# Kernel optimization log

Hardware: AMD Instinct MI355X
Metric: run time of the kernel (lower is better)

The kernel has to match this reference:

```python
import jax, jax.numpy as jnp
import numpy as np

N_NODES = 50000


def gcn_layer(x, W, b, src, dst, norm):
    # x: [N, Fin] -> [N, Fout]; PyG GCNConv: x' = D^-1/2 (A+I) D^-1/2 (x W) + b
    h = x @ W
    msg = h[src] * norm[:, None]              # gather + scale per edge (incl. self loops)
    out = jax.ops.segment_sum(msg, dst, num_segments=N_NODES)
    return out + b


def setup_inputs() -> dict:
    key = jax.random.key(0)
    ks = jax.random.split(key, 12)
    F_in, F_hid, T, E = 128, 128, 10, 1600000
    features = jax.random.normal(ks[0], (N_NODES, F_in), dtype=jnp.float32)
    edges = jax.random.randint(ks[1], (2, E), 0, N_NODES, dtype=jnp.int64)
    s = 1.0 / np.sqrt(F_in)
    W0 = jax.random.uniform(ks[2], (F_in, F_hid), jnp.float32, -s, s)
    b0 = jnp.zeros((F_hid,), jnp.float32)
    W1 = jax.random.uniform(ks[3], (F_hid, F_hid), jnp.float32, -s, s)
    b1 = jnp.zeros((F_hid,), jnp.float32)
    W2 = jax.random.uniform(ks[4], (F_hid, F_hid), jnp.float32, -s, s)
    b2 = jnp.zeros((F_hid,), jnp.float32)
    Wout = jax.random.uniform(ks[5], (F_hid, T), jnp.float32, -s, s)
    bout = jax.random.uniform(ks[6], (T,), jnp.float32, -s, s)
    return {"features": features, "edges": edges, "W0": W0, "b0": b0,
            "W1": W1, "b1": b1, "W2": W2, "b2": b2, "Wout": Wout, "bout": bout}


def reference(features, edges, W0, b0, W1, b1, W2, b2, Wout, bout):
    # Add self loops once; edge structure shared across layers.
    loop = jnp.arange(N_NODES, dtype=edges.dtype)
    src = jnp.concatenate([edges[0], loop])
    dst = jnp.concatenate([edges[1], loop])
    deg = jax.ops.segment_sum(jnp.ones_like(dst, dtype=features.dtype), dst,
                              num_segments=N_NODES)
    dinv = jnp.where(deg > 0, jax.lax.rsqrt(deg), 0.0)
    norm = dinv[src] * dinv[dst]              # [E + N]

    x = gcn_layer(features, W0, b0, src, dst, norm)
    x = gcn_layer(x, W1, b1, src, dst, norm)
    x = gcn_layer(x, W2, b2, src, dst, norm)

    pooled = jnp.mean(x, axis=0)              # [F_hid]
    logits = pooled @ Wout + bout             # [T]
    return jax.nn.log_softmax(logits, axis=0).reshape(1, -1)
```

## Files before the change

### kernel.cpp

```cpp
#include <hip/hip_runtime.h>


#define FDIM 128
#define HSZ 12500
#define NBG 64
#define NB_V0 512
#define S_FIX 16777216.0f
#define INV_S (1.0f / 16777216.0f)


__global__ void __launch_bounds__(1024)
hist_deg_kernel(const int* __restrict__ edges, int E, int e4, int N,
                int* __restrict__ partial) {
  __shared__ int h[HSZ];
  const int g = blockIdx.x / NBG;
  const int j = blockIdx.x - g * NBG;
  const int lo = g * HSZ;
  const int hi = min(N, lo + HSZ);
  const int hs = hi - lo;
  for (int i = threadIdx.x; i < hs; i += blockDim.x) h[i] = 0;
  __syncthreads();
  const int* dst = edges + E;
  const int4* dst4 = (const int4*)dst;
  for (int i = j * blockDim.x + threadIdx.x; i < e4; i += NBG * blockDim.x) {
    int4 d = dst4[i];
    if (d.x >= lo && d.x < hi) atomicAdd(&h[d.x - lo], 1);
    if (d.y >= lo && d.y < hi) atomicAdd(&h[d.y - lo], 1);
    if (d.z >= lo && d.z < hi) atomicAdd(&h[d.z - lo], 1);
    if (d.w >= lo && d.w < hi) atomicAdd(&h[d.w - lo], 1);
  }
  if (j == 0) {
    for (int e = 4 * e4 + threadIdx.x; e < E; e += blockDim.x) {
      int d = dst[e];
      if (d >= lo && d < hi) atomicAdd(&h[d - lo], 1);
    }
  }
  __syncthreads();
  int* out = partial + (size_t)blockIdx.x * HSZ;
  for (int i = threadIdx.x; i < hs; i += blockDim.x) out[i] = h[i];
}

__global__ void merge_dinv_kernel(const int* __restrict__ partial,
                                  float* __restrict__ dinv, int N) {
  int n = blockIdx.x * blockDim.x + threadIdx.x;
  if (n >= N) return;
  int g = n / HSZ;
  int off = n - g * HSZ;
  const int* p = partial + ((size_t)g * NBG) * HSZ + off;
  int s = 1;
  for (int jj = 0; jj < NBG; ++jj) s += p[(size_t)jj * HSZ];
  dinv[n] = rsqrtf((float)s);
}

__global__ void __launch_bounds__(1024)
hist_u_kernel(const int* __restrict__ edges, int E, int e4, int N,
              const float* __restrict__ w,
              float* __restrict__ partial) {
  __shared__ float h[HSZ];
  const int g = blockIdx.x / NBG;
  const int j = blockIdx.x - g * NBG;
  const int lo = g * HSZ;
  const int hi = min(N, lo + HSZ);
  const int hs = hi - lo;
  for (int i = threadIdx.x; i < hs; i += blockDim.x) h[i] = 0.f;
  __syncthreads();
  const int4* s4 = (const int4*)edges;
  const int4* d4 = (const int4*)(edges + E);
  for (int i = j * blockDim.x + threadIdx.x; i < e4; i += NBG * blockDim.x) {
    int4 s = s4[i];
    int4 d = d4[i];
    if (s.x >= lo && s.x < hi) atomicAdd(&h[s.x - lo], w[d.x]);
    if (s.y >= lo && s.y < hi) atomicAdd(&h[s.y - lo], w[d.y]);
    if (s.z >= lo && s.z < hi) atomicAdd(&h[s.z - lo], w[d.z]);
    if (s.w >= lo && s.w < hi) atomicAdd(&h[s.w - lo], w[d.w]);
  }
  if (j == 0) {
    const int* se = edges; const int* de = edges + E;
    for (int e = 4 * e4 + threadIdx.x; e < E; e += blockDim.x) {
      int s = se[e], d = de[e];
      if (s >= lo && s < hi) atomicAdd(&h[s - lo], w[d]);
    }
  }
  __syncthreads();
  float* out = partial + (size_t)blockIdx.x * HSZ;
  for (int i = threadIdx.x; i < hs; i += blockDim.x) out[i] = h[i];
}

__global__ void __launch_bounds__(256)
merge_u_kernel(const float* __restrict__ partial,
               const float* __restrict__ dinv,
               const float* __restrict__ win,
               float* __restrict__ uout,
               float* __restrict__ wout,
               float* __restrict__ ssump, int N) {
  __shared__ float red[4];
  int n = blockIdx.x * blockDim.x + threadIdx.x;
  float u = 0.f;
  if (n < N) {
    int g = n / HSZ;
    int off = n - g * HSZ;
    const float* p = partial + ((size_t)g * NBG) * HSZ + off;
    float s = 0.f;
    for (int jj = 0; jj < NBG; ++jj) s += p[(size_t)jj * HSZ];
    u = dinv[n] * (s + win[n]);
    if (uout) uout[n] = u;
    if (wout) wout[n] = dinv[n] * u;
  }
  if (ssump) {
    float a = u;
    for (int o = 32; o > 0; o >>= 1) a += __shfl_down(a, o, 64);
    if ((threadIdx.x & 63) == 0) red[threadIdx.x >> 6] = a;
    __syncthreads();
    if (threadIdx.x == 0)
      ssump[blockIdx.x] = red[0] + red[1] + red[2] + red[3];
  }
}

__global__ void v0_kernel(const float* __restrict__ feat,
                          const float* __restrict__ u0,
                          float* __restrict__ v0p, int N) {
  __shared__ float sh[2][FDIM];
  int f = threadIdx.x & (FDIM - 1);
  int r2 = threadIdx.x >> 7;
  float acc = 0.f;
  for (int r = blockIdx.x * 2 + r2; r < N; r += gridDim.x * 2)
    acc += u0[r] * feat[(size_t)r * FDIM + f];
  sh[r2][f] = acc;
  __syncthreads();
  if (r2 == 0) v0p[(size_t)blockIdx.x * FDIM + f] = sh[0][f] + sh[1][f];
}

__global__ void __launch_bounds__(1024)
final_kernel(const float* __restrict__ W0, const float* __restrict__ b0,
             const float* __restrict__ W1, const float* __restrict__ b1,
             const float* __restrict__ W2, const float* __restrict__ b2,
             const float* __restrict__ Wout, const float* __restrict__ bout,
             const float* __restrict__ v0p, int nv0,
             const float* __restrict__ ssumpA,
             const float* __restrict__ ssumpB,
             int nss,
             float* __restrict__ out, int N) {
  __shared__ float Wl[FDIM * FDIM];
  __shared__ float WoL[FDIM * 10];
  __shared__ float va[FDIM], vb[FDIM];
  __shared__ float part[8][FDIM];
  __shared__ float red0[16], red1[16];
  __shared__ float shS1, shS2;
  __shared__ float lg[10];
  const int t = threadIdx.x;
  const int f = t & (FDIM - 1);
  const int sl = t >> 7;

  {
    const float4* w4 = (const float4*)W0;
    float4* l4 = (float4*)Wl;
    #pragma unroll
    for (int i = 0; i < 4; ++i) l4[t + i * 1024] = w4[t + i * 1024];
    if (t < (FDIM * 10) / 4) ((float4*)WoL)[t] = ((const float4*)Wout)[t];
  }
  float acc = 0.f;
  for (int j = sl; j < nv0; j += 8) acc += v0p[(size_t)j * FDIM + f];
  part[sl][f] = acc;
  {
    float a0 = 0.f, a1 = 0.f;
    for (int j = t; j < nss; j += 1024) { a0 += ssumpA[j]; a1 += ssumpB[j]; }
    for (int o = 32; o > 0; o >>= 1) {
      a0 += __shfl_down(a0, o, 64);
      a1 += __shfl_down(a1, o, 64);
    }
    if ((t & 63) == 0) { red0[t >> 6] = a0; red1[t >> 6] = a1; }
  }
  __syncthreads();
  if (sl == 0) {
    float s = 0.f;
    #pragma unroll
    for (int j = 0; j < 8; ++j) s += part[j][f];
    va[f] = s;
  }
  if (t == 0) {
    float x = 0.f, y = 0.f;
    #pragma unroll
    for (int i = 0; i < 16; ++i) { x += red0[i]; y += red1[i]; }
    shS2 = x; shS1 = y;
  }
  __syncthreads();

  acc = 0.f;
  #pragma unroll
  for (int k = 0; k < 16; ++k) {
    int kk = sl * 16 + k;
    acc += va[kk] * Wl[kk * FDIM + f];
  }
  part[sl][f] = acc;
  __syncthreads();
  {
    const float4* w4 = (const float4*)W1;
    float4* l4 = (float4*)Wl;
    #pragma unroll
    for (int i = 0; i < 4; ++i) l4[t + i * 1024] = w4[t + i * 1024];
  }
  if (sl == 0) {
    float s = 0.f;
    #pragma unroll
    for (int j = 0; j < 8; ++j) s += part[j][f];
    vb[f] = s + shS1 * b0[f];
  }
  __syncthreads();

  acc = 0.f;
  #pragma unroll
  for (int k = 0; k < 16; ++k) {
    int kk = sl * 16 + k;
    acc += vb[kk] * Wl[kk * FDIM + f];
  }
  part[sl][f] = acc;
  __syncthreads();
  {
    const float4* w4 = (const float4*)W2;
    float4* l4 = (float4*)Wl;
    #pragma unroll
    for (int i = 0; i < 4; ++i) l4[t + i * 1024] = w4[t + i * 1024];
  }
  if (sl == 0) {
    float s = 0.f;
    #pragma unroll
    for (int j = 0; j < 8; ++j) s += part[j][f];
    va[f] = s + shS2 * b1[f];
  }
  __syncthreads();

  acc = 0.f;
  #pragma unroll
  for (int k = 0; k < 16; ++k) {
    int kk = sl * 16 + k;
    acc += va[kk] * Wl[kk * FDIM + f];
  }
  part[sl][f] = acc;
  __syncthreads();
  if (sl == 0) {
    float s = 0.f;
    #pragma unroll
    for (int j = 0; j < 8; ++j) s += part[j][f];
    vb[f] = s / (float)N + b2[f];
  }
  __syncthreads();

  if (t < 10) {
    float a = 0.f;
    for (int k = 0; k < FDIM; ++k) a += vb[k] * WoL[k * 10 + t];
    lg[t] = a + bout[t];
  }
  __syncthreads();
  if (t == 0) {
    float m = lg[0];
    for (int q = 1; q < 10; ++q) m = fmaxf(m, lg[q]);
    float s = 0.f;
    for (int q = 0; q < 10; ++q) s += expf(lg[q] - m);
    float lse = logf(s);
    for (int q = 0; q < 10; ++q) out[q] = lg[q] - m - lse;
  }
}


__global__ void deg_kernel(const int* __restrict__ edges, int E, int M,
                           int* __restrict__ deg) {
  for (int e = blockIdx.x * blockDim.x + threadIdx.x; e < M;
       e += gridDim.x * blockDim.x) {
    int d = (e < E) ? edges[E + e] : (e - E);
    atomicAdd(&deg[d], 1);
  }
}

__global__ void dinv_kernel(const int* __restrict__ deg,
                            float* __restrict__ dinv, int N) {
  int i = blockIdx.x * blockDim.x + threadIdx.x;
  if (i < N) {
    float d = (float)deg[i];
    dinv[i] = (d > 0.f) ? rsqrtf(d) : 0.f;
  }
}

__global__ void upass_kernel(const int* __restrict__ edges, int E, int M,
                             const float* __restrict__ dinv,
                             const int* __restrict__ uin_q,
                             int* __restrict__ uout_q) {
  for (int e = blockIdx.x * blockDim.x + threadIdx.x; e < M;
       e += gridDim.x * blockDim.x) {
    int s, d;
    if (e < E) { s = edges[e]; d = edges[E + e]; }
    else       { s = e - E;    d = s; }
    float v = dinv[s] * dinv[d];
    if (uin_q) v *= (float)uin_q[d] * INV_S;
    atomicAdd(&uout_q[s], __float2int_rn(v * S_FIX));
  }
}

__global__ void sums_kernel(const int* __restrict__ u2q,
                            const int* __restrict__ u1q,
                            float* __restrict__ ssump, int N) {
  __shared__ float red[8];
  int i = blockIdx.x * blockDim.x + threadIdx.x;
  float a = 0.f, b = 0.f;
  if (i < N) { a = (float)u2q[i] * INV_S; b = (float)u1q[i] * INV_S; }
  for (int o = 32; o > 0; o >>= 1) {
    a += __shfl_down(a, o, 64);
    b += __shfl_down(b, o, 64);
  }
  if ((threadIdx.x & 63) == 0) {
    red[(threadIdx.x >> 6) * 2] = a;
    red[(threadIdx.x >> 6) * 2 + 1] = b;
  }
  __syncthreads();
  if (threadIdx.x == 0) {
    ssump[blockIdx.x] = red[0] + red[2] + red[4] + red[6];
    ssump[gridDim.x + blockIdx.x] = red[1] + red[3] + red[5] + red[7];
  }
}

__global__ void v0_fallback_kernel(const float* __restrict__ feat,
                                   const int* __restrict__ u0q,
                                   float* __restrict__ v0p, int N) {
  __shared__ float sh[2][FDIM];
  int f = threadIdx.x & (FDIM - 1);
  int r2 = threadIdx.x >> 7;
  float acc = 0.f;
  for (int r = blockIdx.x * 2 + r2; r < N; r += gridDim.x * 2)
    acc += ((float)u0q[r] * INV_S) * feat[(size_t)r * FDIM + f];
  sh[r2][f] = acc;
  __syncthreads();
  if (r2 == 0) v0p[(size_t)blockIdx.x * FDIM + f] = sh[0][f] + sh[1][f];
}


extern "C" void kernel_launch(void* const* d_in, const int* in_sizes, int n_in,
                              void* d_out, int out_size, void* d_ws, size_t ws_size,
                              hipStream_t stream) {
  const float* feat = (const float*)d_in[0];
  const int*   edges = (const int*)d_in[1];
  const float* W0 = (const float*)d_in[2];
  const float* b0 = (const float*)d_in[3];
  const float* W1 = (const float*)d_in[4];
  const float* b1 = (const float*)d_in[5];
  const float* W2 = (const float*)d_in[6];
  const float* b2 = (const float*)d_in[7];
  const float* Wout = (const float*)d_in[8];
  const float* bout = (const float*)d_in[9];

  const int N = in_sizes[0] / FDIM;
  const int E = in_sizes[1] / 2;
  const int NG = (N + HSZ - 1) / HSZ;
  const int e4 = ((E & 3) == 0) ? (E >> 2) : 0;
  const int mergeGrid = (N + 255) / 256;

  char* ws = (char*)d_ws;
  size_t nb = ((size_t)N * 4 + 511) & ~(size_t)511;
  size_t partB = ((size_t)NG * NBG * HSZ * 4 + 511) & ~(size_t)511;
  size_t v0pB = (size_t)NB_V0 * FDIM * 4;
  size_t ssB = ((size_t)mergeGrid * 4 + 511) & ~(size_t)511;
  size_t need = partB + 4 * nb + v0pB + 2 * ssB;

  if (ws_size >= need) {
    char* p = ws;
    void*  part = (void*)p;        p += partB;
    float* dinv = (float*)p;       p += nb;
    float* w2   = (float*)p;       p += nb;
    float* w1   = (float*)p;       p += nb;
    float* u0   = (float*)p;       p += nb;
    float* v0p  = (float*)p;       p += v0pB;
    float* ssA  = (float*)p;       p += ssB;
    float* ssB_ = (float*)p;

    hist_deg_kernel<<<NG * NBG, 1024, 0, stream>>>(edges, E, e4, N, (int*)part);
    merge_dinv_kernel<<<mergeGrid, 256, 0, stream>>>((const int*)part, dinv, N);
    hist_u_kernel<<<NG * NBG, 1024, 0, stream>>>(edges, E, e4, N, dinv, (float*)part);
    merge_u_kernel<<<mergeGrid, 256, 0, stream>>>((const float*)part, dinv, dinv,
                                                  nullptr, w2, ssA, N);
    hist_u_kernel<<<NG * NBG, 1024, 0, stream>>>(edges, E, e4, N, w2, (float*)part);
    merge_u_kernel<<<mergeGrid, 256, 0, stream>>>((const float*)part, dinv, w2,
                                                  nullptr, w1, ssB_, N);
    hist_u_kernel<<<NG * NBG, 1024, 0, stream>>>(edges, E, e4, N, w1, (float*)part);
    merge_u_kernel<<<mergeGrid, 256, 0, stream>>>((const float*)part, dinv, w1,
                                                  u0, nullptr, nullptr, N);
    v0_kernel<<<NB_V0, 256, 0, stream>>>(feat, u0, v0p, N);
    final_kernel<<<1, 1024, 0, stream>>>(W0, b0, W1, b1, W2, b2, Wout, bout,
                                         v0p, NB_V0, ssA, ssB_, mergeGrid,
                                         (float*)d_out, N);
  } else {
    const int M = E + N;
    int*   deg  = (int*)(ws);
    float* dinv = (float*)(ws + nb);
    int*   u2q  = (int*)(ws + 2 * nb);
    int*   u1q  = (int*)(ws + 3 * nb);
    int*   u0q  = (int*)(ws + 4 * nb);
    float* v0p  = (float*)(ws + 5 * nb);
    float* ssp  = (float*)(ws + 5 * nb + v0pB);

    hipMemsetAsync(ws, 0, 5 * nb, stream);

    deg_kernel<<<2048, 256, 0, stream>>>(edges, E, M, deg);
    dinv_kernel<<<mergeGrid, 256, 0, stream>>>(deg, dinv, N);
    upass_kernel<<<2048, 256, 0, stream>>>(edges, E, M, dinv, nullptr, u2q);
    upass_kernel<<<2048, 256, 0, stream>>>(edges, E, M, dinv, u2q, u1q);
    upass_kernel<<<2048, 256, 0, stream>>>(edges, E, M, dinv, u1q, u0q);
    sums_kernel<<<mergeGrid, 256, 0, stream>>>(u2q, u1q, ssp, N);
    v0_fallback_kernel<<<NB_V0, 256, 0, stream>>>(feat, u0q, v0p, N);
    final_kernel<<<1, 1024, 0, stream>>>(W0, b0, W1, b1, W2, b2, Wout, bout,
                                         v0p, NB_V0, ssp, ssp + mergeGrid,
                                         mergeGrid, (float*)d_out, N);
  }
}
```

Before: 125.3 us.

## Bucket edges by source once and run per-bucket shared-memory passes

Adds a count/scan/scatter preprocessing that groups edges into 256 source buckets of 196 nodes, packing local source and destination into one int. Each of the three propagation passes then reads only its own bucket and accumulates into small per-wave shared histograms, which replaces the full edge rescans and 64-way partial merges. The last pass also folds in the weighted feature reduction (v0). This trades three extra preprocessing kernels and an E-sized bucket buffer for far less edge traffic and no separate merge kernels. It requires N up to 65535 and enough workspace, and falls back to the old path otherwise.

```diff
diff --git a/kernel.cpp b/kernel.cpp
--- a/kernel.cpp
+++ b/kernel.cpp
@@ -4,9 +4,125 @@
 #define FDIM 128
 #define HSZ 12500
 #define NBG 64
-#define NB_V0 512
+#define BSZ 196
+#define NBKT 256
+#define SCB 256
+#define STG 6400
 #define S_FIX 16777216.0f
 #define INV_S (1.0f / 16777216.0f)
+
+
+__global__ void __launch_bounds__(256)
+count_kernel(const int* __restrict__ edges, int E, int e4,
+             int* __restrict__ blockCnt) {
+  __shared__ int cnt[NBKT];
+  for (int i = threadIdx.x; i < NBKT; i += 256) cnt[i] = 0;
+  __syncthreads();
+  const int per4 = (e4 + SCB - 1) / SCB;
+  const int i0 = blockIdx.x * per4;
+  const int i1 = min(e4, i0 + per4);
+  const int4* s4 = (const int4*)edges;
+  for (int i = i0 + threadIdx.x; i < i1; i += 256) {
+    int4 s = s4[i];
+    atomicAdd(&cnt[s.x / BSZ], 1);
+    atomicAdd(&cnt[s.y / BSZ], 1);
+    atomicAdd(&cnt[s.z / BSZ], 1);
+    atomicAdd(&cnt[s.w / BSZ], 1);
+  }
+  if (blockIdx.x == 0) {
+    for (int e = 4 * e4 + threadIdx.x; e < E; e += 256)
+      atomicAdd(&cnt[edges[e] / BSZ], 1);
+  }
+  __syncthreads();
+  for (int i = threadIdx.x; i < NBKT; i += 256)
+    blockCnt[blockIdx.x * NBKT + i] = cnt[i];
+}
+
+__global__ void __launch_bounds__(256)
+scan_kernel(const int* __restrict__ blockCnt, int* __restrict__ blockOff,
+            int* __restrict__ meta) {
+  __shared__ int tot[NBKT];
+  __shared__ int base[NBKT];
+  const int k = threadIdx.x;
+  int run = 0;
+  for (int b = 0; b < SCB; ++b) {
+    int v = blockCnt[b * NBKT + k];
+    blockOff[b * NBKT + k] = run;
+    run += v;
+  }
+  tot[k] = run;
+  __syncthreads();
+  if (k == 0) {
+    int acc = 0;
+    for (int q = 0; q < NBKT; ++q) { base[q] = acc; acc += tot[q]; }
+  }
+  __syncthreads();
+  for (int b = 0; b < SCB; ++b)
+    blockOff[b * NBKT + k] += base[k];
+  meta[k] = base[k];
+  meta[NBKT + k] = tot[k];
+}
+
+__global__ void __launch_bounds__(256)
+scatter_kernel(const int* __restrict__ edges, int E, int e4,
+               const int* __restrict__ blockOff, int* __restrict__ bucket) {
+  __shared__ int cnt[NBKT];
+  __shared__ int off2[NBKT];
+  __shared__ int offRun[NBKT];
+  __shared__ int stg[STG];
+  const int per4 = (e4 + SCB - 1) / SCB;
+  const int i0 = blockIdx.x * per4;
+  const int i1 = min(e4, i0 + per4);
+  const int4* s4 = (const int4*)edges;
+  const int4* d4 = (const int4*)(edges + E);
+
+  for (int i = threadIdx.x; i < NBKT; i += 256) cnt[i] = 0;
+  __syncthreads();
+  for (int i = i0 + threadIdx.x; i < i1; i += 256) {
+    int4 s = s4[i];
+    atomicAdd(&cnt[s.x / BSZ], 1);
+    atomicAdd(&cnt[s.y / BSZ], 1);
+    atomicAdd(&cnt[s.z / BSZ], 1);
+    atomicAdd(&cnt[s.w / BSZ], 1);
+  }
+  if (blockIdx.x == 0) {
+    for (int e = 4 * e4 + threadIdx.x; e < E; e += 256)
+      atomicAdd(&cnt[edges[e] / BSZ], 1);
+  }
+  __syncthreads();
+  if (threadIdx.x == 0) {
+    int acc = 0;
+    for (int q = 0; q < NBKT; ++q) { off2[q] = acc; offRun[q] = acc; acc += cnt[q]; }
+  }
+  __syncthreads();
+  for (int i = i0 + threadIdx.x; i < i1; i += 256) {
+    int4 s = s4[i];
+    int4 d = d4[i];
+    int b, p;
+    b = s.x / BSZ; p = atomicAdd(&offRun[b], 1); stg[p] = ((s.x - b * BSZ) << 16) | d.x;
+    b = s.y / BSZ; p = atomicAdd(&offRun[b], 1); stg[p] = ((s.y - b * BSZ) << 16) | d.y;
+    b = s.z / BSZ; p = atomicAdd(&offRun[b], 1); stg[p] = ((s.z - b * BSZ) << 16) | d.z;
+    b = s.w / BSZ; p = atomicAdd(&offRun[b], 1); stg[p] = ((s.w - b * BSZ) << 16) | d.w;
+  }
+  if (blockIdx.x == 0) {
+    for (int e = 4 * e4 + threadIdx.x; e < E; e += 256) {
+      int s = edges[e], d = edges[E + e];
+      int b = s / BSZ;
+      int p = atomicAdd(&offRun[b], 1);
+      stg[p] = ((s - b * BSZ) << 16) | d;
+    }
+  }
+  __syncthreads();
+  const int wv = threadIdx.x >> 6;
+  const int ln = threadIdx.x & 63;
+  for (int k = wv; k < NBKT; k += 4) {
+    const int len = cnt[k];
+    const int lb = off2[k];
+    const int gb = blockOff[blockIdx.x * NBKT + k];
+    for (int i = ln; i < len; i += 64)
+      bucket[gb + i] = stg[lb + i];
+  }
+}
 
 
 __global__ void __launch_bounds__(1024)
@@ -52,83 +168,77 @@
   dinv[n] = rsqrtf((float)s);
 }
 
+
 __global__ void __launch_bounds__(1024)
-hist_u_kernel(const int* __restrict__ edges, int E, int e4, int N,
-              const float* __restrict__ w,
-              float* __restrict__ partial) {
-  __shared__ float h[HSZ];
-  const int g = blockIdx.x / NBG;
-  const int j = blockIdx.x - g * NBG;
-  const int lo = g * HSZ;
-  const int hi = min(N, lo + HSZ);
-  const int hs = hi - lo;
-  for (int i = threadIdx.x; i < hs; i += blockDim.x) h[i] = 0.f;
-  __syncthreads();
-  const int4* s4 = (const int4*)edges;
-  const int4* d4 = (const int4*)(edges + E);
-  for (int i = j * blockDim.x + threadIdx.x; i < e4; i += NBG * blockDim.x) {
-    int4 s = s4[i];
-    int4 d = d4[i];
-    if (s.x >= lo && s.x < hi) atomicAdd(&h[s.x - lo], w[d.x]);
-    if (s.y >= lo && s.y < hi) atomicAdd(&h[s.y - lo], w[d.y]);
-    if (s.z >= lo && s.z < hi) atomicAdd(&h[s.z - lo], w[d.z]);
-    if (s.w >= lo && s.w < hi) atomicAdd(&h[s.w - lo], w[d.w]);
-  }
-  if (j == 0) {
-    const int* se = edges; const int* de = edges + E;
-    for (int e = 4 * e4 + threadIdx.x; e < E; e += blockDim.x) {
-      int s = se[e], d = de[e];
-      if (s >= lo && s < hi) atomicAdd(&h[s - lo], w[d]);
-    }
-  }
-  __syncthreads();
-  float* out = partial + (size_t)blockIdx.x * HSZ;
-  for (int i = threadIdx.x; i < hs; i += blockDim.x) out[i] = h[i];
-}
-
-__global__ void __launch_bounds__(256)
-merge_u_kernel(const float* __restrict__ partial,
-               const float* __restrict__ dinv,
-               const float* __restrict__ win,
-               float* __restrict__ uout,
-               float* __restrict__ wout,
-               float* __restrict__ ssump, int N) {
-  __shared__ float red[4];
-  int n = blockIdx.x * blockDim.x + threadIdx.x;
+pass_kernel(const int* __restrict__ bucket, const int* __restrict__ meta,
+            const float* __restrict__ dinv, const float* __restrict__ win,
+            float* __restrict__ wout, float* __restrict__ ssump,
+            const float* __restrict__ feat, float* __restrict__ v0p,
+            int N, int doV0) {
+  __shared__ float uacc[16][200];
+  __shared__ float ul[BSZ];
+  __shared__ float red[16];
+  __shared__ float partS[8][FDIM];
+  const int t = threadIdx.x;
+  const int wv = t >> 6;
+  const int b = blockIdx.x;
+  const int n0 = b * BSZ;
+  const int ns = min(BSZ, N - n0);
+
+  for (int i = t; i < 16 * 200; i += 1024)
+    ((float*)uacc)[i] = 0.f;
+  __syncthreads();
+
+  const int base = meta[b];
+  const int end = base + meta[NBKT + b];
+  for (int i = base + t; i < end; i += 1024) {
+    int p = bucket[i];
+    atomicAdd(&uacc[wv][p >> 16], win[p & 0xFFFF]);
+  }
+  __syncthreads();
+
   float u = 0.f;
-  if (n < N) {
-    int g = n / HSZ;
-    int off = n - g * HSZ;
-    const float* p = partial + ((size_t)g * NBG) * HSZ + off;
-    float s = 0.f;
-    for (int jj = 0; jj < NBG; ++jj) s += p[(size_t)jj * HSZ];
+  if (t < ns) {
+    float s = 0.f;
+    #pragma unroll
+    for (int k = 0; k < 16; ++k) s += uacc[k][t];
+    int n = n0 + t;
     u = dinv[n] * (s + win[n]);
-    if (uout) uout[n] = u;
     if (wout) wout[n] = dinv[n] * u;
+    ul[t] = u;
+  } else if (t < BSZ) {
+    ul[t] = 0.f;
   }
   if (ssump) {
     float a = u;
     for (int o = 32; o > 0; o >>= 1) a += __shfl_down(a, o, 64);
-    if ((threadIdx.x & 63) == 0) red[threadIdx.x >> 6] = a;
+    if ((t & 63) == 0) red[wv] = a;
     __syncthreads();
-    if (threadIdx.x == 0)
-      ssump[blockIdx.x] = red[0] + red[1] + red[2] + red[3];
-  }
-}
-
-__global__ void v0_kernel(const float* __restrict__ feat,
-                          const float* __restrict__ u0,
-                          float* __restrict__ v0p, int N) {
-  __shared__ float sh[2][FDIM];
-  int f = threadIdx.x & (FDIM - 1);
-  int r2 = threadIdx.x >> 7;
-  float acc = 0.f;
-  for (int r = blockIdx.x * 2 + r2; r < N; r += gridDim.x * 2)
-    acc += u0[r] * feat[(size_t)r * FDIM + f];
-  sh[r2][f] = acc;
-  __syncthreads();
-  if (r2 == 0) v0p[(size_t)blockIdx.x * FDIM + f] = sh[0][f] + sh[1][f];
-}
+    if (t == 0) {
+      float s = 0.f;
+      #pragma unroll
+      for (int k = 0; k < 16; ++k) s += red[k];
+      ssump[b] = s;
+    }
+  }
+  if (doV0) {
+    __syncthreads();
+    const int f = t & (FDIM - 1);
+    const int r8 = t >> 7;
+    float acc = 0.f;
+    for (int r = r8; r < ns; r += 8)
+      acc += ul[r] * feat[(size_t)(n0 + r) * FDIM + f];
+    partS[r8][f] = acc;
+    __syncthreads();
+    if (r8 == 0) {
+      float s = 0.f;
+      #pragma unroll
+      for (int k = 0; k < 8; ++k) s += partS[k][f];
+      v0p[(size_t)b * FDIM + f] = s;
+    }
+  }
+}
+
 
 __global__ void __launch_bounds__(1024)
 final_kernel(const float* __restrict__ W0, const float* __restrict__ b0,
@@ -262,73 +372,87 @@
 }
 
 
-__global__ void deg_kernel(const int* __restrict__ edges, int E, int M,
-                           int* __restrict__ deg) {
-  for (int e = blockIdx.x * blockDim.x + threadIdx.x; e < M;
-       e += gridDim.x * blockDim.x) {
-    int d = (e < E) ? edges[E + e] : (e - E);
-    atomicAdd(&deg[d], 1);
-  }
-}
-
-__global__ void dinv_kernel(const int* __restrict__ deg,
-                            float* __restrict__ dinv, int N) {
-  int i = blockIdx.x * blockDim.x + threadIdx.x;
-  if (i < N) {
-    float d = (float)deg[i];
-    dinv[i] = (d > 0.f) ? rsqrtf(d) : 0.f;
-  }
-}
-
-__global__ void upass_kernel(const int* __restrict__ edges, int E, int M,
-                             const float* __restrict__ dinv,
-                             const int* __restrict__ uin_q,
-                             int* __restrict__ uout_q) {
-  for (int e = blockIdx.x * blockDim.x + threadIdx.x; e < M;
-       e += gridDim.x * blockDim.x) {
-    int s, d;
-    if (e < E) { s = edges[e]; d = edges[E + e]; }
-    else       { s = e - E;    d = s; }
-    float v = dinv[s] * dinv[d];
-    if (uin_q) v *= (float)uin_q[d] * INV_S;
-    atomicAdd(&uout_q[s], __float2int_rn(v * S_FIX));
-  }
-}
-
-__global__ void sums_kernel(const int* __restrict__ u2q,
-                            const int* __restrict__ u1q,
-                            float* __restrict__ ssump, int N) {
-  __shared__ float red[8];
-  int i = blockIdx.x * blockDim.x + threadIdx.x;
-  float a = 0.f, b = 0.f;
-  if (i < N) { a = (float)u2q[i] * INV_S; b = (float)u1q[i] * INV_S; }
-  for (int o = 32; o > 0; o >>= 1) {
-    a += __shfl_down(a, o, 64);
-    b += __shfl_down(b, o, 64);
-  }
-  if ((threadIdx.x & 63) == 0) {
-    red[(threadIdx.x >> 6) * 2] = a;
-    red[(threadIdx.x >> 6) * 2 + 1] = b;
-  }
-  __syncthreads();
-  if (threadIdx.x == 0) {
-    ssump[blockIdx.x] = red[0] + red[2] + red[4] + red[6];
-    ssump[gridDim.x + blockIdx.x] = red[1] + red[3] + red[5] + red[7];
-  }
-}
-
-__global__ void v0_fallback_kernel(const float* __restrict__ feat,
-                                   const int* __restrict__ u0q,
-                                   float* __restrict__ v0p, int N) {
-  __shared__ float sh[2][FDIM];
+__global__ void __launch_bounds__(1024)
+hist_u_kernel(const int* __restrict__ edges, int E, int e4, int N,
+              const float* __restrict__ w,
+              float* __restrict__ partial) {
+  __shared__ float h[HSZ];
+  const int g = blockIdx.x / NBG;
+  const int j = blockIdx.x - g * NBG;
+  const int lo = g * HSZ;
+  const int hi = min(N, lo + HSZ);
+  const int hs = hi - lo;
+  for (int i = threadIdx.x; i < hs; i += blockDim.x) h[i] = 0.f;
+  __syncthreads();
+  const int4* s4 = (const int4*)edges;
+  const int4* d4 = (const int4*)(edges + E);
+  for (int i = j * blockDim.x + threadIdx.x; i < e4; i += NBG * blockDim.x) {
+    int4 s = s4[i];
+    int4 d = d4[i];
+    if (s.x >= lo && s.x < hi) atomicAdd(&h[s.x - lo], w[d.x]);
+    if (s.y >= lo && s.y < hi) atomicAdd(&h[s.y - lo], w[d.y]);
+    if (s.z >= lo && s.z < hi) atomicAdd(&h[s.z - lo], w[d.z]);
+    if (s.w >= lo && s.w < hi) atomicAdd(&h[s.w - lo], w[d.w]);
+  }
+  if (j == 0) {
+    const int* se = edges; const int* de = edges + E;
+    for (int e = 4 * e4 + threadIdx.x; e < E; e += blockDim.x) {
+      int s = se[e], d = de[e];
+      if (s >= lo && s < hi) atomicAdd(&h[s - lo], w[d]);
+    }
+  }
+  __syncthreads();
+  float* out = partial + (size_t)blockIdx.x * HSZ;
+  for (int i = threadIdx.x; i < hs; i += blockDim.x) out[i] = h[i];
+}
+
+__global__ void __launch_bounds__(256)
+merge_u_kernel(const float* __restrict__ partial,
+               const float* __restrict__ dinv,
+               const float* __restrict__ win,
+               float* __restrict__ uout,
+               float* __restrict__ wout,
+               float* __restrict__ ssump, int N) {
+  __shared__ float red[4];
+  int n = blockIdx.x * blockDim.x + threadIdx.x;
+  float u = 0.f;
+  if (n < N) {
+    int g = n / HSZ;
+    int off = n - g * HSZ;
+    const float* p = partial + ((size_t)g * NBG) * HSZ + off;
+    float s = 0.f;
+    for (int jj = 0; jj < NBG; ++jj) s += p[(size_t)jj * HSZ];
+    u = dinv[n] * (s + win[n]);
+    if (uout) uout[n] = u;
+    if (wout) wout[n] = dinv[n] * u;
+  }
+  if (ssump) {
+    float a = u;
+    for (int o = 32; o > 0; o >>= 1) a += __shfl_down(a, o, 64);
+    if ((threadIdx.x & 63) == 0) red[threadIdx.x >> 6] = a;
+    __syncthreads();
+    if (threadIdx.x == 0)
+      ssump[blockIdx.x] = red[0] + red[1] + red[2] + red[3];
+  }
+}
+
+__global__ void __launch_bounds__(1024)
+v0_kernel(const float* __restrict__ feat, const float* __restrict__ u0,
+          float* __restrict__ v0p, int N) {
+  __shared__ float sh[8][FDIM];
   int f = threadIdx.x & (FDIM - 1);
-  int r2 = threadIdx.x >> 7;
+  int r8 = threadIdx.x >> 7;
   float acc = 0.f;
-  for (int r = blockIdx.x * 2 + r2; r < N; r += gridDim.x * 2)
-    acc += ((float)u0q[r] * INV_S) * feat[(size_t)r * FDIM + f];
-  sh[r2][f] = acc;
-  __syncthreads();
-  if (r2 == 0) v0p[(size_t)blockIdx.x * FDIM + f] = sh[0][f] + sh[1][f];
+  for (int r = blockIdx.x * 8 + r8; r < N; r += 128 * 8)
+    acc += u0[r] * feat[(size_t)r * FDIM + f];
+  sh[r8][f] = acc;
+  __syncthreads();
+  if (r8 == 0) {
+    float s = acc;
+    #pragma unroll
+    for (int k = 1; k < 8; ++k) s += sh[k][f];
+    v0p[(size_t)blockIdx.x * FDIM + f] = s;
+  }
 }
 
 
@@ -348,64 +472,66 @@
 
   const int N = in_sizes[0] / FDIM;
   const int E = in_sizes[1] / 2;
-  const int NG = (N + HSZ - 1) / HSZ;
-  const int e4 = ((E & 3) == 0) ? (E >> 2) : 0;
+  const int e4 = E >> 2;
   const int mergeGrid = (N + 255) / 256;
 
   char* ws = (char*)d_ws;
   size_t nb = ((size_t)N * 4 + 511) & ~(size_t)511;
-  size_t partB = ((size_t)NG * NBG * HSZ * 4 + 511) & ~(size_t)511;
-  size_t v0pB = (size_t)NB_V0 * FDIM * 4;
-  size_t ssB = ((size_t)mergeGrid * 4 + 511) & ~(size_t)511;
-  size_t need = partB + 4 * nb + v0pB + 2 * ssB;
-
-  if (ws_size >= need) {
-    char* p = ws;
-    void*  part = (void*)p;        p += partB;
-    float* dinv = (float*)p;       p += nb;
-    float* w2   = (float*)p;       p += nb;
-    float* w1   = (float*)p;       p += nb;
-    float* u0   = (float*)p;       p += nb;
-    float* v0p  = (float*)p;       p += v0pB;
-    float* ssA  = (float*)p;       p += ssB;
-    float* ssB_ = (float*)p;
-
-    hist_deg_kernel<<<NG * NBG, 1024, 0, stream>>>(edges, E, e4, N, (int*)part);
+  size_t partB = ((size_t)4 * NBG * HSZ * 4 + 511) & ~(size_t)511;
+  size_t v0pB = ((size_t)NBKT * FDIM * 4 + 511) & ~(size_t)511;
+  size_t ssBsz = ((size_t)NBKT * 4 + 511) & ~(size_t)511;
+  size_t bktB = ((size_t)E * 4 + 511) & ~(size_t)511;
+  size_t cntB = (size_t)SCB * NBKT * 4;
+  size_t need = partB + 4 * nb + v0pB + 2 * ssBsz + bktB + 2 * cntB + 4096;
+
+  char* p = ws;
+  float* part = (float*)p;       p += partB;
+  float* dinv = (float*)p;       p += nb;
+  float* w2   = (float*)p;       p += nb;
+  float* w1   = (float*)p;       p += nb;
+  float* u0   = (float*)p;       p += nb;
+  float* v0p  = (float*)p;       p += v0pB;
+  float* ssA  = (float*)p;       p += ssBsz;
+  float* ssB_ = (float*)p;       p += ssBsz;
+  int* bucket = (int*)p;         p += bktB;
+  int* blockCnt = (int*)p;       p += cntB;
+  int* blockOff = (int*)p;       p += cntB;
+  int* meta   = (int*)p;
+
+  const int perBlkEdges = ((e4 + SCB - 1) / SCB) * 4 + 4;
+  const bool bucketOK = (ws_size >= need) && (N <= NBKT * BSZ) &&
+                        (N <= 65535) && (perBlkEdges <= STG);
+
+  if (bucketOK) {
+    count_kernel<<<SCB, 256, 0, stream>>>(edges, E, e4, blockCnt);
+    scan_kernel<<<1, NBKT, 0, stream>>>(blockCnt, blockOff, meta);
+    scatter_kernel<<<SCB, 256, 0, stream>>>(edges, E, e4, blockOff, bucket);
+    hist_deg_kernel<<<4 * NBG, 1024, 0, stream>>>(edges, E, e4, N, (int*)part);
     merge_dinv_kernel<<<mergeGrid, 256, 0, stream>>>((const int*)part, dinv, N);
-    hist_u_kernel<<<NG * NBG, 1024, 0, stream>>>(edges, E, e4, N, dinv, (float*)part);
-    merge_u_kernel<<<mergeGrid, 256, 0, stream>>>((const float*)part, dinv, dinv,
-                                                  nullptr, w2, ssA, N);
-    hist_u_kernel<<<NG * NBG, 1024, 0, stream>>>(edges, E, e4, N, w2, (float*)part);
-    merge_u_kernel<<<mergeGrid, 256, 0, stream>>>((const float*)part, dinv, w2,
-                                                  nullptr, w1, ssB_, N);
-    hist_u_kernel<<<NG * NBG, 1024, 0, stream>>>(edges, E, e4, N, w1, (float*)part);
-    merge_u_kernel<<<mergeGrid, 256, 0, stream>>>((const float*)part, dinv, w1,
-                                                  u0, nullptr, nullptr, N);
-    v0_kernel<<<NB_V0, 256, 0, stream>>>(feat, u0, v0p, N);
+    pass_kernel<<<NBKT, 1024, 0, stream>>>(bucket, meta, dinv, dinv,
+                                           w2, ssA, nullptr, nullptr, N, 0);
+    pass_kernel<<<NBKT, 1024, 0, stream>>>(bucket, meta, dinv, w2,
+                                           w1, ssB_, nullptr, nullptr, N, 0);
+    pass_kernel<<<NBKT, 1024, 0, stream>>>(bucket, meta, dinv, w1,
+                                           nullptr, nullptr, feat, v0p, N, 1);
     final_kernel<<<1, 1024, 0, stream>>>(W0, b0, W1, b1, W2, b2, Wout, bout,
-                                         v0p, NB_V0, ssA, ssB_, mergeGrid,
+                                         v0p, NBKT, ssA, ssB_, NBKT,
                                          (float*)d_out, N);
   } else {
-    const int M = E + N;
-    int*   deg  = (int*)(ws);
-    float* dinv = (float*)(ws + nb);
-    int*   u2q  = (int*)(ws + 2 * nb);
-    int*   u1q  = (int*)(ws + 3 * nb);
-    int*   u0q  = (int*)(ws + 4 * nb);
-    float* v0p  = (float*)(ws + 5 * nb);
-    float* ssp  = (float*)(ws + 5 * nb + v0pB);
-
-    hipMemsetAsync(ws, 0, 5 * nb, stream);
-
-    deg_kernel<<<2048, 256, 0, stream>>>(edges, E, M, deg);
-    dinv_kernel<<<mergeGrid, 256, 0, stream>>>(deg, dinv, N);
-    upass_kernel<<<2048, 256, 0, stream>>>(edges, E, M, dinv, nullptr, u2q);
-    upass_kernel<<<2048, 256, 0, stream>>>(edges, E, M, dinv, u2q, u1q);
-    upass_kernel<<<2048, 256, 0, stream>>>(edges, E, M, dinv, u1q, u0q);
-    sums_kernel<<<mergeGrid, 256, 0, stream>>>(u2q, u1q, ssp, N);
-    v0_fallback_kernel<<<NB_V0, 256, 0, stream>>>(feat, u0q, v0p, N);
+    hist_deg_kernel<<<4 * NBG, 1024, 0, stream>>>(edges, E, e4, N, (int*)part);
+    merge_dinv_kernel<<<mergeGrid, 256, 0, stream>>>((const int*)part, dinv, N);
+    hist_u_kernel<<<4 * NBG, 1024, 0, stream>>>(edges, E, e4, N, dinv, part);
+    merge_u_kernel<<<mergeGrid, 256, 0, stream>>>(part, dinv, dinv,
+                                                  nullptr, w2, ssA, N);
+    hist_u_kernel<<<4 * NBG, 1024, 0, stream>>>(edges, E, e4, N, w2, part);
+    merge_u_kernel<<<mergeGrid, 256, 0, stream>>>(part, dinv, w2,
+                                                  nullptr, w1, ssB_, N);
+    hist_u_kernel<<<4 * NBG, 1024, 0, stream>>>(edges, E, e4, N, w1, part);
+    merge_u_kernel<<<mergeGrid, 256, 0, stream>>>(part, dinv, w1,
+                                                  u0, nullptr, nullptr, N);
+    v0_kernel<<<128, 1024, 0, stream>>>(feat, u0, v0p, N);
     final_kernel<<<1, 1024, 0, stream>>>(W0, b0, W1, b1, W2, b2, Wout, bout,
-                                         v0p, NB_V0, ssp, ssp + mergeGrid,
-                                         mergeGrid, (float*)d_out, N);
-  }
-}
+                                         v0p, 128, ssA, ssB_, mergeGrid,
+                                         (float*)d_out, N);
+  }
+}
```

Result: slower. 142.4 us (+13.6%).
